# Kernel tuning notes

Measured on AMD Instinct MI355X. Metric: run time of the kernel, lower is better.

Reference implementation:

```python
import jax, jax.numpy as jnp
import numpy as np

IMG_H, IMG_W = 1024, 1024
TWO_PI = 2.0 * np.pi


def _pe_encoding(coords_norm, gauss):
    # coords_norm: [..., 2] in [0,1]
    c = 2.0 * coords_norm - 1.0
    c = (c @ gauss) * TWO_PI  # [..., num_pos_feats]
    return jnp.concatenate([jnp.sin(c), jnp.cos(c)], axis=-1)  # [..., embed_dim]


def setup_inputs() -> dict:
    key = jax.random.key(0)
    ks = jax.random.split(key, 9)
    B, N, D = 2048, 128, 256
    points = jax.random.uniform(ks[0], (B, N, 2), dtype=jnp.float32) * 1024.0
    labels = jax.random.randint(ks[1], (B, N), -1, 2, dtype=jnp.int32)  # {-1,0,1}
    boxes = jax.random.uniform(ks[2], (B, 4), dtype=jnp.float32) * 1024.0
    gauss = jax.random.normal(ks[3], (2, D // 2), dtype=jnp.float32)  # scale=1.0
    pe0 = jax.random.normal(ks[4], (D,), dtype=jnp.float32)
    pe1 = jax.random.normal(ks[5], (D,), dtype=jnp.float32)
    pe2 = jax.random.normal(ks[6], (D,), dtype=jnp.float32)
    pe3 = jax.random.normal(ks[7], (D,), dtype=jnp.float32)
    nap = jax.random.normal(ks[8], (D,), dtype=jnp.float32)
    return {"points": points, "labels": labels, "boxes": boxes, "gauss": gauss,
            "pe0": pe0, "pe1": pe1, "pe2": pe2, "pe3": pe3, "nap": nap}


def reference(points, labels, boxes, gauss, pe0, pe1, pe2, pe3, nap):
    inv_size = jnp.asarray([1.0 / IMG_W, 1.0 / IMG_H], dtype=points.dtype)

    # --- _embed_points (pad=False since boxes are given) ---
    p = (points + 0.5) * inv_size  # normalize x by W, y by H
    point_emb = _pe_encoding(p, gauss)  # [B, N, D]
    lab = labels[..., None]  # [B, N, 1]
    delta = jnp.where(lab == -1, nap,
             jnp.where(lab == 1, pe0,
              jnp.where(lab == 0, pe1, jnp.zeros_like(nap))))
    point_emb = point_emb + delta

    # --- _embed_boxes ---
    b = (boxes + 0.5).reshape(boxes.shape[0], 2, 2) * inv_size
    corner_emb = _pe_encoding(b, gauss)  # [B, 2, D]
    corner_emb = corner_emb + jnp.stack([pe2, pe3], axis=0)  # broadcast over B
    box_emb = jnp.mean(corner_emb, axis=1, keepdims=True)  # [B, 1, D]

    combined = jnp.concatenate([point_emb, box_emb], axis=1)  # [B, N+1, D]
    return jnp.mean(combined, axis=1, keepdims=True)  # [B, 1, D]
```

## Files before the change

### kernel.cpp

```cpp
#include <hip/hip_runtime.h>
#include <math.h>


#define N_PTS 128
#define NFEAT 128

__device__ __forceinline__ float sin2pi(float t) { return __builtin_amdgcn_sinf(t); }
__device__ __forceinline__ float cos2pi(float t) { return __builtin_amdgcn_cosf(t); }
__device__ __forceinline__ float fract_(float t) { return __builtin_amdgcn_fractf(t); }

__global__ __launch_bounds__(128)
void prompt_encoder_kernel(const float* __restrict__ points,
                           const int*   __restrict__ labels,
                           const float* __restrict__ boxes,
                           const float* __restrict__ gauss,
                           const float* __restrict__ pe0,
                           const float* __restrict__ pe1,
                           const float* __restrict__ pe2,
                           const float* __restrict__ pe3,
                           const float* __restrict__ nap,
                           float* __restrict__ out)
{
    const int b = blockIdx.x;
    const int j = threadIdx.x;

    __shared__ float sc[2 * N_PTS];
    __shared__ int   scnt[3];

    {
        float2 p = ((const float2*)(points + (size_t)b * N_PTS * 2))[j];
        sc[2 * j]     = (p.x + 0.5f) * (1.0f / 512.0f) - 1.0f;
        sc[2 * j + 1] = (p.y + 0.5f) * (1.0f / 512.0f) - 1.0f;
        if (j < 3) scnt[j] = 0;
    }
    __syncthreads();
    {
        int lab = labels[(size_t)b * N_PTS + j];
        atomicAdd(&scnt[lab + 1], 1);
    }

    const float g0 = gauss[j];
    const float g1 = gauss[NFEAT + j];

    __syncthreads();

    float ssum = 0.0f, csum = 0.0f;
    #pragma unroll 8
    for (int n = 0; n < N_PTS; ++n) {
        float cx = sc[2 * n];
        float cy = sc[2 * n + 1];
        float t  = fract_(cx * g0 + cy * g1);
        ssum += sin2pi(t);
        csum += cos2pi(t);
    }

    float cm1 = (float)scnt[0];
    float c0  = (float)scnt[1];
    float cp1 = (float)scnt[2];

    const int ds = j;
    const int dc = j + NFEAT;
    float dels = cm1 * nap[ds] + cp1 * pe0[ds] + c0 * pe1[ds];
    float delc = cm1 * nap[dc] + cp1 * pe0[dc] + c0 * pe1[dc];

    float4 bx  = ((const float4*)boxes)[b];
    float c0x = (bx.x + 0.5f) * (1.0f / 512.0f) - 1.0f;
    float c0y = (bx.y + 0.5f) * (1.0f / 512.0f) - 1.0f;
    float c1x = (bx.z + 0.5f) * (1.0f / 512.0f) - 1.0f;
    float c1y = (bx.w + 0.5f) * (1.0f / 512.0f) - 1.0f;
    float t0 = fract_(c0x * g0 + c0y * g1);
    float t1 = fract_(c1x * g0 + c1y * g1);
    float boxs = 0.5f * ((sin2pi(t0) + pe2[ds]) + (sin2pi(t1) + pe3[ds]));
    float boxc = 0.5f * ((cos2pi(t0) + pe2[dc]) + (cos2pi(t1) + pe3[dc]));

    const float inv_np1 = 1.0f / (float)(N_PTS + 1);
    out[(size_t)b * 256 + ds] = (ssum + dels + boxs) * inv_np1;
    out[(size_t)b * 256 + dc] = (csum + delc + boxc) * inv_np1;
}

extern "C" void kernel_launch(void* const* d_in, const int* in_sizes, int n_in,
                              void* d_out, int out_size, void* d_ws, size_t ws_size,
                              hipStream_t stream) {
    const float* points = (const float*)d_in[0];
    const int*   labels = (const int*)d_in[1];
    const float* boxes  = (const float*)d_in[2];
    const float* gauss  = (const float*)d_in[3];
    const float* pe0    = (const float*)d_in[4];
    const float* pe1    = (const float*)d_in[5];
    const float* pe2    = (const float*)d_in[6];
    const float* pe3    = (const float*)d_in[7];
    const float* nap    = (const float*)d_in[8];
    float* out = (float*)d_out;

    const int B = in_sizes[2] / 4;

    prompt_encoder_kernel<<<B, 128, 0, stream>>>(points, labels, boxes, gauss,
                                                 pe0, pe1, pe2, pe3, nap, out);
}
```

Measured before the change: 14.97 us.

## Split point loop across two thread halves with shared-memory reduction

Doubles the block to 256 threads. Each half of the block processes half of the 128 points for every feature, and the partial sin and cos sums are combined through shared memory. Each thread then writes one output element, so the delta and box terms are computed per output rather than twice per thread. This shortens the serial transcendental loop per thread and adds parallelism, at the cost of an extra barrier, more shared memory and more threads per block.

```diff
diff --git a/kernel.cpp b/kernel.cpp
--- a/kernel.cpp
+++ b/kernel.cpp
@@ -9,7 +9,7 @@
 __device__ __forceinline__ float cos2pi(float t) { return __builtin_amdgcn_cosf(t); }
 __device__ __forceinline__ float fract_(float t) { return __builtin_amdgcn_fractf(t); }
 
-__global__ __launch_bounds__(128)
+__global__ __launch_bounds__(256)
 void prompt_encoder_kernel(const float* __restrict__ points,
                            const int*   __restrict__ labels,
                            const float* __restrict__ boxes,
@@ -21,61 +21,68 @@
                            const float* __restrict__ nap,
                            float* __restrict__ out)
 {
-    const int b = blockIdx.x;
-    const int j = threadIdx.x;
+    const int b   = blockIdx.x;
+    const int tid = threadIdx.x;
+    const int j   = tid & (NFEAT - 1);
+    const int h   = tid >> 7;
 
-    __shared__ float sc[2 * N_PTS];
-    __shared__ int   scnt[3];
+    __shared__ float2 sc[N_PTS];
+    __shared__ float  psin[2 * NFEAT];
+    __shared__ float  pcos[2 * NFEAT];
+    __shared__ int    scnt[4];
 
-    {
-        float2 p = ((const float2*)(points + (size_t)b * N_PTS * 2))[j];
-        sc[2 * j]     = (p.x + 0.5f) * (1.0f / 512.0f) - 1.0f;
-        sc[2 * j + 1] = (p.y + 0.5f) * (1.0f / 512.0f) - 1.0f;
-        if (j < 3) scnt[j] = 0;
+    if (tid < 4) scnt[tid] = 0;
+    if (tid < N_PTS) {
+        float2 p = ((const float2*)(points + (size_t)b * N_PTS * 2))[tid];
+        sc[tid] = make_float2((p.x + 0.5f) * (1.0f / 512.0f) - 1.0f,
+                              (p.y + 0.5f) * (1.0f / 512.0f) - 1.0f);
     }
     __syncthreads();
-    {
-        int lab = labels[(size_t)b * N_PTS + j];
+
+    if (tid < N_PTS) {
+        int lab = labels[(size_t)b * N_PTS + tid];
         atomicAdd(&scnt[lab + 1], 1);
     }
 
     const float g0 = gauss[j];
     const float g1 = gauss[NFEAT + j];
 
+    float ss = 0.0f, cs = 0.0f;
+    const int n0 = h * (N_PTS / 2);
+    #pragma unroll 8
+    for (int n = 0; n < N_PTS / 2; ++n) {
+        float2 c = sc[n0 + n];
+        float  t = fract_(fmaf(c.x, g0, c.y * g1));
+        ss += sin2pi(t);
+        cs += cos2pi(t);
+    }
+    psin[tid] = ss;
+    pcos[tid] = cs;
     __syncthreads();
 
-    float ssum = 0.0f, csum = 0.0f;
-    #pragma unroll 8
-    for (int n = 0; n < N_PTS; ++n) {
-        float cx = sc[2 * n];
-        float cy = sc[2 * n + 1];
-        float t  = fract_(cx * g0 + cy * g1);
-        ssum += sin2pi(t);
-        csum += cos2pi(t);
-    }
+    const int d  = tid;
+    const int jj = d & (NFEAT - 1);
+    float sum = (d < NFEAT) ? (psin[jj] + psin[NFEAT + jj])
+                            : (pcos[jj] + pcos[NFEAT + jj]);
 
     float cm1 = (float)scnt[0];
-    float c0  = (float)scnt[1];
+    float c0n = (float)scnt[1];
     float cp1 = (float)scnt[2];
+    float delv = cm1 * nap[d] + cp1 * pe0[d] + c0n * pe1[d];
 
-    const int ds = j;
-    const int dc = j + NFEAT;
-    float dels = cm1 * nap[ds] + cp1 * pe0[ds] + c0 * pe1[ds];
-    float delc = cm1 * nap[dc] + cp1 * pe0[dc] + c0 * pe1[dc];
+    float gg0 = gauss[jj];
+    float gg1 = gauss[NFEAT + jj];
+    float4 bx = ((const float4*)boxes)[b];
+    float t0 = fract_(fmaf((bx.x + 0.5f) * (1.0f / 512.0f) - 1.0f, gg0,
+                           ((bx.y + 0.5f) * (1.0f / 512.0f) - 1.0f) * gg1));
+    float t1 = fract_(fmaf((bx.z + 0.5f) * (1.0f / 512.0f) - 1.0f, gg0,
+                           ((bx.w + 0.5f) * (1.0f / 512.0f) - 1.0f) * gg1));
+    float tr0, tr1;
+    if (d < NFEAT) { tr0 = sin2pi(t0); tr1 = sin2pi(t1); }
+    else           { tr0 = cos2pi(t0); tr1 = cos2pi(t1); }
+    float box = 0.5f * ((tr0 + pe2[d]) + (tr1 + pe3[d]));
 
-    float4 bx  = ((const float4*)boxes)[b];
-    float c0x = (bx.x + 0.5f) * (1.0f / 512.0f) - 1.0f;
-    float c0y = (bx.y + 0.5f) * (1.0f / 512.0f) - 1.0f;
-    float c1x = (bx.z + 0.5f) * (1.0f / 512.0f) - 1.0f;
-    float c1y = (bx.w + 0.5f) * (1.0f / 512.0f) - 1.0f;
-    float t0 = fract_(c0x * g0 + c0y * g1);
-    float t1 = fract_(c1x * g0 + c1y * g1);
-    float boxs = 0.5f * ((sin2pi(t0) + pe2[ds]) + (sin2pi(t1) + pe3[ds]));
-    float boxc = 0.5f * ((cos2pi(t0) + pe2[dc]) + (cos2pi(t1) + pe3[dc]));
-
-    const float inv_np1 = 1.0f / (float)(N_PTS + 1);
-    out[(size_t)b * 256 + ds] = (ssum + dels + boxs) * inv_np1;
-    out[(size_t)b * 256 + dc] = (csum + delc + boxc) * inv_np1;
+    out[(size_t)b * 256 + d] = (sum + delv + box) * (1.0f / (float)(N_PTS + 1));
 }
 
 extern "C" void kernel_launch(void* const* d_in, const int* in_sizes, int n_in,
@@ -94,6 +101,6 @@
 
     const int B = in_sizes[2] / 4;
 
-    prompt_encoder_kernel<<<B, 128, 0, stream>>>(points, labels, boxes, gauss,
+    prompt_encoder_kernel<<<B, 256, 0, stream>>>(points, labels, boxes, gauss,
                                                  pe0, pe1, pe2, pe3, nap, out);
 }
```

Result: faster. 14.51 us (-3.0%).
